# Kernel tuning notes

Hardware: AMD Instinct MI355X
Metric: run time of the kernel (lower is better)

Reference implementation:

```python
import jax, jax.numpy as jnp
import numpy as np
from jax import lax

PS = 16            # patch_size
QT = 0.7           # quality_threshold
SAP = 0.8          # strong_aug_prob
PDP = 0.1          # patch_drop_prob


def setup_inputs() -> dict:
    key = jax.random.key(0)
    ks = jax.random.split(key, 10)
    B, C, H, W = 32, 1, 1024, 1024
    pH, pW = H // PS, W // PS
    img = jax.random.uniform(ks[0], (B, C, H, W), jnp.float32)
    noise = jax.random.normal(ks[1], (B, C, H, W), jnp.float32)
    r_strong = jax.random.uniform(ks[2], (pH, pW), jnp.float32)
    r_drop = jax.random.uniform(ks[3], (pH, pW), jnp.float32)
    r_else = jax.random.uniform(ks[4], (pH, pW), jnp.float32)
    bright_f = jax.random.uniform(ks[5], (pH, pW), jnp.float32, minval=0.7, maxval=1.3)
    contrast_f = jax.random.uniform(ks[6], (pH, pW), jnp.float32, minval=0.7, maxval=1.3)
    slight_f = jax.random.uniform(ks[7], (pH, pW), jnp.float32, minval=0.9, maxval=1.1)
    aug_choice = jax.random.randint(ks[8], (pH, pW), 0, 4, jnp.int32)
    slight_choice = jax.random.randint(ks[9], (pH, pW), 0, 2, jnp.int32)
    return dict(img=img, noise=noise, r_strong=r_strong, r_drop=r_drop,
                r_else=r_else, bright_f=bright_f, contrast_f=contrast_f,
                slight_f=slight_f, aug_choice=aug_choice, slight_choice=slight_choice)


def _forward(img, noise, r_strong, r_drop, r_else, bright_f, contrast_f,
             slight_f, aug_choice, slight_choice):
    B, C, H, W = img.shape
    pH, pW = H // PS, W // PS
    # (B, C, pH, pW, PS, PS) patch view
    p6 = img.reshape(B, C, pH, PS, pW, PS).transpose(0, 1, 2, 4, 3, 5)
    flat = p6.reshape(B, C, pH, pW, PS * PS)
    mean_i = flat.mean(-1)
    var = flat.var(-1, ddof=1)          # torch .var/.std are unbiased
    std = jnp.sqrt(var)
    intensity_q = 1.0 - 2.0 * jnp.abs(mean_i - 0.5)
    quality = (std + intensity_q + var) / 3.0   # (B, C, pH, pW)
    q = quality.squeeze(1).mean(0)               # batch-mean quality per patch (pH, pW)

    low = q < QT
    strong = low & (r_strong < SAP)
    drop = low & (q < 0.3) & (r_drop < PDP)
    els = (~low) & (r_else < 0.3)

    # per-patch action code: 0=identity, 1=noise, 2=blur, 3=brightness,
    # 4=contrast, 5=slight_noise, 6=slight_brightness, 7=drop
    code = jnp.where(strong, aug_choice + 1, 0)
    code = jnp.where(els, slight_choice + 5, code)
    code = jnp.where(drop, 7, code)

    up = lambda m: jnp.repeat(jnp.repeat(m, PS, axis=0), PS, axis=1)  # (pH,pW)->(H,W)
    cu = up(code)[None, None]

    # candidate augmented images (patches are disjoint, so compute globally + mask)
    noise_img = jnp.clip(img + noise * 0.1, 0.0, 1.0)
    # per-patch 3x3 avg pool with zero padding confined to each patch
    blur6 = lax.reduce_window(p6, 0.0, lax.add,
                              (1, 1, 1, 1, 3, 3), (1, 1, 1, 1, 1, 1),
                              [(0, 0)] * 4 + [(1, 1), (1, 1)]) / 9.0
    blur_img = blur6.transpose(0, 1, 2, 4, 3, 5).reshape(B, C, H, W)
    bright_img = jnp.clip(img * up(bright_f)[None, None], 0.0, 1.0)
    m_pp = up(p6.mean(axis=(0, 1, 4, 5)))[None, None]   # patch.mean() over B,C,PS,PS
    cf = up(contrast_f)[None, None]
    contrast_img = jnp.clip((img - m_pp) * cf + m_pp, 0.0, 1.0)
    snoise_img = jnp.clip(img + noise * 0.05, 0.0, 1.0)
    sbright_img = jnp.clip(img * up(slight_f)[None, None], 0.0, 1.0)

    out = jnp.where(cu == 1, noise_img, img)
    out = jnp.where(cu == 2, blur_img, out)
    out = jnp.where(cu == 3, bright_img, out)
    out = jnp.where(cu == 4, contrast_img, out)
    out = jnp.where(cu == 5, snoise_img, out)
    out = jnp.where(cu == 6, sbright_img, out)
    out = jnp.where(cu == 7, 0.0, out)
    return out


def reference(img, noise, r_strong, r_drop, r_else, bright_f, contrast_f,
              slight_f, aug_choice, slight_choice):
    return _forward(img, noise, r_strong, r_drop, r_else, bright_f,
                    contrast_f, slight_f, aug_choice, slight_choice)
```

## Files before the change

kernel.cpp:

```cpp
#include <hip/hip_runtime.h>
#include <math.h>

#define PS 16
#define PH 64
#define PWD 64
#define NB 32
#define IW 1024
#define IH 1024
#define NPATCH (PH*PWD)

__device__ __forceinline__ float clamp01(float v) {
    return fminf(fmaxf(v, 0.0f), 1.0f);
}

__global__ __launch_bounds__(256) void stats_kernel(const float* __restrict__ img,
                                                    float* __restrict__ ws_mean,
                                                    float* __restrict__ ws_qual) {
    const int blk = blockIdx.x;
    const int b  = blk >> 6;
    const int ph = blk & 63;
    const int t  = threadIdx.x;

    size_t base = ((size_t)b * IH + (size_t)ph * PS) * IW + (size_t)t * 4;
    float s = 0.0f, ss = 0.0f;
#pragma unroll
    for (int i = 0; i < PS; ++i) {
        float4 v = *(const float4*)(img + base + (size_t)i * IW);
        s  += v.x + v.y + v.z + v.w;
        ss += v.x * v.x + v.y * v.y + v.z * v.z + v.w * v.w;
    }
    s  += __shfl_xor(s, 1);  ss += __shfl_xor(ss, 1);
    s  += __shfl_xor(s, 2);  ss += __shfl_xor(ss, 2);

    if ((t & 3) == 0) {
        float mean = s * (1.0f / 256.0f);
        float var  = (ss - s * s * (1.0f / 256.0f)) * (1.0f / 255.0f);
        var = fmaxf(var, 0.0f);
        float sd   = sqrtf(var);
        float iq   = 1.0f - 2.0f * fabsf(mean - 0.5f);
        float qual = (sd + iq + var) * (1.0f / 3.0f);
        int p = ph * PWD + (t >> 2);
        ws_mean[b * NPATCH + p] = mean;
        ws_qual[b * NPATCH + p] = qual;
    }
}

__global__ __launch_bounds__(256) void decide_kernel(const float* __restrict__ ws_mean,
                                                     const float* __restrict__ ws_qual,
                                                     const float* __restrict__ r_strong,
                                                     const float* __restrict__ r_drop,
                                                     const float* __restrict__ r_else,
                                                     const float* __restrict__ bright_f,
                                                     const float* __restrict__ contrast_f,
                                                     const float* __restrict__ slight_f,
                                                     const int* __restrict__ aug_choice,
                                                     const int* __restrict__ slight_choice,
                                                     int* __restrict__ ws_op,
                                                     float* __restrict__ ws_a,
                                                     float* __restrict__ ws_b) {
    int p = blockIdx.x * 256 + threadIdx.x;
    if (p >= NPATCH) return;
    float qs = 0.0f, ms = 0.0f;
    for (int b = 0; b < NB; ++b) {
        qs += ws_qual[b * NPATCH + p];
        ms += ws_mean[b * NPATCH + p];
    }
    float q   = qs * (1.0f / (float)NB);
    float mpp = ms * (1.0f / (float)NB);

    bool low    = q < 0.7f;
    bool strong = low && (r_strong[p] < 0.8f);
    bool drop   = low && (q < 0.3f) && (r_drop[p] < 0.1f);
    bool els    = (!low) && (r_else[p] < 0.3f);

    int code = strong ? (aug_choice[p] + 1) : 0;
    if (els)  code = slight_choice[p] + 5;
    if (drop) code = 7;

    int op = 0; float a = 0.0f, bb = 0.0f;
    switch (code) {
        case 1: op = 1; a = 0.1f;  break;
        case 5: op = 1; a = 0.05f; break;
        case 2: op = 2; break;
        case 3: op = 3; a = bright_f[p]; bb = 0.0f; break;
        case 6: op = 3; a = slight_f[p]; bb = 0.0f; break;
        case 4: { op = 3; float cf = contrast_f[p];
                  a = cf; bb = mpp - mpp * cf; break; }
        case 7: op = 4; break;
        default: break;
    }
    ws_op[p] = op; ws_a[p] = a; ws_b[p] = bb;
}

__global__ __launch_bounds__(256) void apply_kernel(const float* __restrict__ img,
                                                    const float* __restrict__ noise,
                                                    const int* __restrict__ ws_op,
                                                    const float* __restrict__ ws_a,
                                                    const float* __restrict__ ws_b,
                                                    float* __restrict__ out) {
    const int blk = blockIdx.x;
    const int b  = blk >> 6;
    const int ph = blk & 63;
    const int t  = threadIdx.x;

    const size_t base = ((size_t)b * IH + (size_t)ph * PS) * IW + (size_t)t * 4;

    const int pp = ph * PWD + (t >> 2);
    const int op = ws_op[pp];
    const float a  = ws_a[pp];
    const float bb = ws_b[pp];

    if (op != 2) {
#pragma unroll 4
        for (int i = 0; i < PS; ++i) {
            float4 x = *(const float4*)(img + base + (size_t)i * IW);
            float4 y;
            if (op == 1) {
                float4 n = *(const float4*)(noise + base + (size_t)i * IW);
                y.x = clamp01(fmaf(n.x, a, x.x));
                y.y = clamp01(fmaf(n.y, a, x.y));
                y.z = clamp01(fmaf(n.z, a, x.z));
                y.w = clamp01(fmaf(n.w, a, x.w));
            } else if (op == 3) {
                y.x = clamp01(fmaf(x.x, a, bb));
                y.y = clamp01(fmaf(x.y, a, bb));
                y.z = clamp01(fmaf(x.z, a, bb));
                y.w = clamp01(fmaf(x.w, a, bb));
            } else if (op == 4) {
                y.x = y.y = y.z = y.w = 0.0f;
            } else {
                y = x;
            }
            *(float4*)(out + base + (size_t)i * IW) = y;
        }
    }
    if (op == 2) {
        const bool left_edge  = (t & 3) == 0;
        const bool right_edge = (t & 3) == 3;
        float4 prev = make_float4(0.f, 0.f, 0.f, 0.f);
        float4 cur  = *(const float4*)(img + base);
        float4 next;
        for (int i = 0; i < PS; ++i) {
            if (i < PS - 1) next = *(const float4*)(img + base + (size_t)(i + 1) * IW);
            else            next = make_float4(0.f, 0.f, 0.f, 0.f);
            float4 v;
            v.x = prev.x + cur.x + next.x;
            v.y = prev.y + cur.y + next.y;
            v.z = prev.z + cur.z + next.z;
            v.w = prev.w + cur.w + next.w;
            float left  = __shfl_up(v.w, 1);
            float right = __shfl_down(v.x, 1);
            if (left_edge)  left  = 0.0f;
            if (right_edge) right = 0.0f;
            float4 y;
            y.x = (left + v.x + v.y) * (1.0f / 9.0f);
            y.y = (v.x + v.y + v.z) * (1.0f / 9.0f);
            y.z = (v.y + v.z + v.w) * (1.0f / 9.0f);
            y.w = (v.z + v.w + right) * (1.0f / 9.0f);
            *(float4*)(out + base + (size_t)i * IW) = y;
            prev = cur; cur = next;
        }
    }
}

extern "C" void kernel_launch(void* const* d_in, const int* in_sizes, int n_in,
                              void* d_out, int out_size, void* d_ws, size_t ws_size,
                              hipStream_t stream) {
    const float* img        = (const float*)d_in[0];
    const float* noise      = (const float*)d_in[1];
    const float* r_strong   = (const float*)d_in[2];
    const float* r_drop     = (const float*)d_in[3];
    const float* r_else     = (const float*)d_in[4];
    const float* bright_f   = (const float*)d_in[5];
    const float* contrast_f = (const float*)d_in[6];
    const float* slight_f   = (const float*)d_in[7];
    const int*   aug_choice    = (const int*)d_in[8];
    const int*   slight_choice = (const int*)d_in[9];
    float* out = (float*)d_out;

    float* ws      = (float*)d_ws;
    float* ws_mean = ws;
    float* ws_qual = ws + NB * NPATCH;
    int*   ws_op   = (int*)(ws + 2 * NB * NPATCH);
    float* ws_a    = ws + 2 * NB * NPATCH + NPATCH;
    float* ws_b    = ws + 2 * NB * NPATCH + 2 * NPATCH;

    stats_kernel<<<NB * PH, 256, 0, stream>>>(img, ws_mean, ws_qual);
    decide_kernel<<<NPATCH / 256, 256, 0, stream>>>(ws_mean, ws_qual,
        r_strong, r_drop, r_else, bright_f, contrast_f, slight_f,
        aug_choice, slight_choice, ws_op, ws_a, ws_b);
    apply_kernel<<<NB * PH, 256, 0, stream>>>(img, noise, ws_op, ws_a, ws_b, out);
}
```

Measured before the change: 375.4 us.

## Fuse per-patch decision into apply kernel and unify blur/pointwise loop

Removes the separate decide kernel. Each apply block now recomputes the batch-mean quality and action code for its 64 patches into shared memory, then synchronises before use. The per-row loop is merged so every op shares one streaming load path with a next-row prefetch. This saves a kernel launch and the global round trip for op/a/b. In exchange, each of the 32 batch blocks per patch row repeats the 32-deep reduction, adding redundant reads and a barrier ahead of the main stream.

```diff
diff --git a/kernel.cpp b/kernel.cpp
--- a/kernel.cpp
+++ b/kernel.cpp
@@ -45,104 +45,83 @@
     }
 }
 
-__global__ __launch_bounds__(256) void decide_kernel(const float* __restrict__ ws_mean,
-                                                     const float* __restrict__ ws_qual,
-                                                     const float* __restrict__ r_strong,
-                                                     const float* __restrict__ r_drop,
-                                                     const float* __restrict__ r_else,
-                                                     const float* __restrict__ bright_f,
-                                                     const float* __restrict__ contrast_f,
-                                                     const float* __restrict__ slight_f,
-                                                     const int* __restrict__ aug_choice,
-                                                     const int* __restrict__ slight_choice,
-                                                     int* __restrict__ ws_op,
-                                                     float* __restrict__ ws_a,
-                                                     float* __restrict__ ws_b) {
-    int p = blockIdx.x * 256 + threadIdx.x;
-    if (p >= NPATCH) return;
-    float qs = 0.0f, ms = 0.0f;
-    for (int b = 0; b < NB; ++b) {
-        qs += ws_qual[b * NPATCH + p];
-        ms += ws_mean[b * NPATCH + p];
-    }
-    float q   = qs * (1.0f / (float)NB);
-    float mpp = ms * (1.0f / (float)NB);
-
-    bool low    = q < 0.7f;
-    bool strong = low && (r_strong[p] < 0.8f);
-    bool drop   = low && (q < 0.3f) && (r_drop[p] < 0.1f);
-    bool els    = (!low) && (r_else[p] < 0.3f);
-
-    int code = strong ? (aug_choice[p] + 1) : 0;
-    if (els)  code = slight_choice[p] + 5;
-    if (drop) code = 7;
-
-    int op = 0; float a = 0.0f, bb = 0.0f;
-    switch (code) {
-        case 1: op = 1; a = 0.1f;  break;
-        case 5: op = 1; a = 0.05f; break;
-        case 2: op = 2; break;
-        case 3: op = 3; a = bright_f[p]; bb = 0.0f; break;
-        case 6: op = 3; a = slight_f[p]; bb = 0.0f; break;
-        case 4: { op = 3; float cf = contrast_f[p];
-                  a = cf; bb = mpp - mpp * cf; break; }
-        case 7: op = 4; break;
-        default: break;
-    }
-    ws_op[p] = op; ws_a[p] = a; ws_b[p] = bb;
-}
-
 __global__ __launch_bounds__(256) void apply_kernel(const float* __restrict__ img,
                                                     const float* __restrict__ noise,
-                                                    const int* __restrict__ ws_op,
-                                                    const float* __restrict__ ws_a,
-                                                    const float* __restrict__ ws_b,
+                                                    const float* __restrict__ ws_mean,
+                                                    const float* __restrict__ ws_qual,
+                                                    const float* __restrict__ r_strong,
+                                                    const float* __restrict__ r_drop,
+                                                    const float* __restrict__ r_else,
+                                                    const float* __restrict__ bright_f,
+                                                    const float* __restrict__ contrast_f,
+                                                    const float* __restrict__ slight_f,
+                                                    const int* __restrict__ aug_choice,
+                                                    const int* __restrict__ slight_choice,
                                                     float* __restrict__ out) {
+    __shared__ int   s_op[PWD];
+    __shared__ float s_a[PWD];
+    __shared__ float s_b[PWD];
+
     const int blk = blockIdx.x;
     const int b  = blk >> 6;
     const int ph = blk & 63;
     const int t  = threadIdx.x;
 
+    if (t < PWD) {
+        const int p = ph * PWD + t;
+        float qs = 0.0f, ms = 0.0f;
+#pragma unroll 8
+        for (int bi = 0; bi < NB; ++bi) {
+            qs += ws_qual[bi * NPATCH + p];
+            ms += ws_mean[bi * NPATCH + p];
+        }
+        float q   = qs * (1.0f / (float)NB);
+        float mpp = ms * (1.0f / (float)NB);
+
+        bool low    = q < 0.7f;
+        bool strong = low && (r_strong[p] < 0.8f);
+        bool drop   = low && (q < 0.3f) && (r_drop[p] < 0.1f);
+        bool els    = (!low) && (r_else[p] < 0.3f);
+
+        int code = strong ? (aug_choice[p] + 1) : 0;
+        if (els)  code = slight_choice[p] + 5;
+        if (drop) code = 7;
+
+        int op = 0; float a = 0.0f, bb = 0.0f;
+        switch (code) {
+            case 1: op = 1; a = 0.1f;  break;
+            case 5: op = 1; a = 0.05f; break;
+            case 2: op = 2; break;
+            case 3: op = 3; a = bright_f[p]; break;
+            case 6: op = 3; a = slight_f[p]; break;
+            case 4: { op = 3; float cf = contrast_f[p];
+                      a = cf; bb = mpp - mpp * cf; break; }
+            case 7: op = 4; break;
+            default: break;
+        }
+        s_op[t] = op; s_a[t] = a; s_b[t] = bb;
+    }
+    __syncthreads();
+
+    const int pw = t >> 2;
+    const int op   = s_op[pw];
+    const float a  = s_a[pw];
+    const float bb = s_b[pw];
+    const bool left_edge  = (t & 3) == 0;
+    const bool right_edge = (t & 3) == 3;
+
     const size_t base = ((size_t)b * IH + (size_t)ph * PS) * IW + (size_t)t * 4;
 
-    const int pp = ph * PWD + (t >> 2);
-    const int op = ws_op[pp];
-    const float a  = ws_a[pp];
-    const float bb = ws_b[pp];
+    float4 prev = make_float4(0.f, 0.f, 0.f, 0.f);
+    float4 cur  = *(const float4*)(img + base);
+    float4 next;
+#pragma unroll 4
+    for (int i = 0; i < PS; ++i) {
+        if (i < PS - 1) next = *(const float4*)(img + base + (size_t)(i + 1) * IW);
+        else            next = make_float4(0.f, 0.f, 0.f, 0.f);
 
-    if (op != 2) {
-#pragma unroll 4
-        for (int i = 0; i < PS; ++i) {
-            float4 x = *(const float4*)(img + base + (size_t)i * IW);
-            float4 y;
-            if (op == 1) {
-                float4 n = *(const float4*)(noise + base + (size_t)i * IW);
-                y.x = clamp01(fmaf(n.x, a, x.x));
-                y.y = clamp01(fmaf(n.y, a, x.y));
-                y.z = clamp01(fmaf(n.z, a, x.z));
-                y.w = clamp01(fmaf(n.w, a, x.w));
-            } else if (op == 3) {
-                y.x = clamp01(fmaf(x.x, a, bb));
-                y.y = clamp01(fmaf(x.y, a, bb));
-                y.z = clamp01(fmaf(x.z, a, bb));
-                y.w = clamp01(fmaf(x.w, a, bb));
-            } else if (op == 4) {
-                y.x = y.y = y.z = y.w = 0.0f;
-            } else {
-                y = x;
-            }
-            *(float4*)(out + base + (size_t)i * IW) = y;
-        }
-    }
-    if (op == 2) {
-        const bool left_edge  = (t & 3) == 0;
-        const bool right_edge = (t & 3) == 3;
-        float4 prev = make_float4(0.f, 0.f, 0.f, 0.f);
-        float4 cur  = *(const float4*)(img + base);
-        float4 next;
-        for (int i = 0; i < PS; ++i) {
-            if (i < PS - 1) next = *(const float4*)(img + base + (size_t)(i + 1) * IW);
-            else            next = make_float4(0.f, 0.f, 0.f, 0.f);
+        float4 y;
+        if (op == 2) {
             float4 v;
             v.x = prev.x + cur.x + next.x;
             v.y = prev.y + cur.y + next.y;
@@ -152,14 +131,28 @@
             float right = __shfl_down(v.x, 1);
             if (left_edge)  left  = 0.0f;
             if (right_edge) right = 0.0f;
-            float4 y;
             y.x = (left + v.x + v.y) * (1.0f / 9.0f);
             y.y = (v.x + v.y + v.z) * (1.0f / 9.0f);
             y.z = (v.y + v.z + v.w) * (1.0f / 9.0f);
             y.w = (v.z + v.w + right) * (1.0f / 9.0f);
-            *(float4*)(out + base + (size_t)i * IW) = y;
-            prev = cur; cur = next;
+        } else if (op == 1) {
+            float4 n = *(const float4*)(noise + base + (size_t)i * IW);
+            y.x = clamp01(fmaf(n.x, a, cur.x));
+            y.y = clamp01(fmaf(n.y, a, cur.y));
+            y.z = clamp01(fmaf(n.z, a, cur.z));
+            y.w = clamp01(fmaf(n.w, a, cur.w));
+        } else if (op == 3) {
+            y.x = clamp01(fmaf(cur.x, a, bb));
+            y.y = clamp01(fmaf(cur.y, a, bb));
+            y.z = clamp01(fmaf(cur.z, a, bb));
+            y.w = clamp01(fmaf(cur.w, a, bb));
+        } else if (op == 4) {
+            y.x = y.y = y.z = y.w = 0.0f;
+        } else {
+            y = cur;
         }
+        *(float4*)(out + base + (size_t)i * IW) = y;
+        prev = cur; cur = next;
     }
 }
 
@@ -181,13 +174,9 @@
     float* ws      = (float*)d_ws;
     float* ws_mean = ws;
     float* ws_qual = ws + NB * NPATCH;
-    int*   ws_op   = (int*)(ws + 2 * NB * NPATCH);
-    float* ws_a    = ws + 2 * NB * NPATCH + NPATCH;
-    float* ws_b    = ws + 2 * NB * NPATCH + 2 * NPATCH;
 
     stats_kernel<<<NB * PH, 256, 0, stream>>>(img, ws_mean, ws_qual);
-    decide_kernel<<<NPATCH / 256, 256, 0, stream>>>(ws_mean, ws_qual,
+    apply_kernel<<<NB * PH, 256, 0, stream>>>(img, noise, ws_mean, ws_qual,
         r_strong, r_drop, r_else, bright_f, contrast_f, slight_f,
-        aug_choice, slight_choice, ws_op, ws_a, ws_b);
-    apply_kernel<<<NB * PH, 256, 0, stream>>>(img, noise, ws_op, ws_a, ws_b, out);
+        aug_choice, slight_choice, out);
 }
```

Measured after the change: 355.1 us. 5.4% less time.
